# Kernel optimization log

Measured on AMD Instinct MI355X. Metric: run time of the kernel, lower is better.

## Reference

```python
import jax, jax.numpy as jnp
import numpy as np

N = 64
H = 256
B = 32768
OFF = N * (N - 1) // 2  # 2016


def _mlp_params(key, dims, scale_out=0.05):
    ps = []
    for i, (din, dout) in enumerate(zip(dims[:-1], dims[1:])):
        key, k = jax.random.split(key)
        s = 1.0 / np.sqrt(din)
        ps.append((jax.random.normal(k, (dout, din), jnp.float32) * s,
                   jnp.zeros((dout,), jnp.float32)))
    return ps, key


def setup_inputs() -> dict:
    key = jax.random.key(0)
    key, k = jax.random.split(key)
    x = jax.random.normal(k, (B, N), jnp.float32)
    dp, key = _mlp_params(key, [N, H, H, N])
    op, key = _mlp_params(key, [N, H, H, OFF])
    (Wd1, bd1), (Wd2, bd2), (Wdo, bdo) = dp
    (Wo1, bo1), (Wo2, bo2), (Woo, boo) = op
    return {"input": x,
            "Wd1": Wd1, "bd1": bd1, "Wd2": Wd2, "bd2": bd2, "Wdo": Wdo, "bdo": bdo,
            "Wo1": Wo1, "bo1": bo1, "Wo2": Wo2, "bo2": bo2, "Woo": Woo, "boo": boo}


def reference(input, Wd1, bd1, Wd2, bd2, Wdo, bdo, Wo1, bo1, Wo2, bo2, Woo, boo):
    x0 = input  # [B, N]
    # diag branch: tanh MLP -> N diagonal elements per sample
    x = jnp.tanh(input @ Wd1.T + bd1)
    x = jnp.tanh(x @ Wd2.T + bd2)
    x = x @ Wdo.T + bdo  # [B, N]
    # offdiag branch: tanh MLP -> N(N-1)/2 strictly-lower-tri elements
    z = jnp.tanh(input @ Wo1.T + bo1)
    z = jnp.tanh(z @ Wo2.T + bo2)
    z = z @ Woo.T + boo  # [B, OFF]
    n = x.shape[-1]
    b = x0.shape[0]
    rows, cols = np.tril_indices(n, k=-1)  # static index arrays
    diag = np.arange(n)
    L = jnp.zeros((b, n, n), x.dtype)
    L = L.at[:, rows, cols].set(z)
    L = L.at[:, diag, diag].set(x)
    # D[i] = (L L^T) x0[i] computed as L @ (L^T @ x0) to avoid n x n matmul
    y = jnp.einsum('bkj,bk->bj', L, x0)
    D = jnp.einsum('bij,bj->bi', L, y)
    return D
```

## Files before the change

kernel.cpp:

```cpp
#include <hip/hip_runtime.h>
#include <math.h>


#define B_TOT 32768
#define NDIM  64
#define HDIM  256
#define OFFD  2016
#define GRP_UNITS 67584
#define GRP_BYTES 135168

typedef __bf16 bf16x8 __attribute__((ext_vector_type(8)));
typedef float  f32x4  __attribute__((ext_vector_type(4)));

__device__ __forceinline__ float fast_tanh(float x) {
  float e = __expf(2.f * x);
  return 1.f - 2.f * __builtin_amdgcn_rcpf(e + 1.f);
}
__device__ __forceinline__ float lane_bcast(float v, int l) {
  return __uint_as_float(__builtin_amdgcn_readlane(__float_as_uint(v), l));
}
__device__ __forceinline__ float bf_lo(unsigned w) { return __uint_as_float(w << 16); }
__device__ __forceinline__ float bf_hi(unsigned w) { return __uint_as_float(w & 0xffff0000u); }
__device__ __forceinline__ unsigned bfbits(float f) {
  __bf16 h = (__bf16)f;
  return (unsigned)__builtin_bit_cast(unsigned short, h);
}
__device__ __forceinline__ int rs_of(int i) {
  const int a3 = i & 3;
  return ((i * (i - 1)) >> 1) + 6 * (i >> 2) + ((a3 == 2) ? 3 : (a3 == 3) ? 5 : 0);
}

__device__ __forceinline__ void gload_lds16(const void* g, void* l) {
  __builtin_amdgcn_global_load_lds(
      (const __attribute__((address_space(1))) unsigned*)g,
      (__attribute__((address_space(3))) unsigned*)l, 16, 0, 0);
}

#define MFMA(A, B, C) __builtin_amdgcn_mfma_f32_16x16x32_bf16((A), (B), (C), 0, 0, 0)
#define SB0() __builtin_amdgcn_sched_barrier(0)
#define GOFF(g, row) (((((g) & ~7) | (((g) & 7) ^ ((row) & 7)))) << 4)

__device__ __forceinline__ void cast_range(const float* __restrict__ s,
                                           __bf16* __restrict__ d, int n) {
  int i = blockIdx.x * blockDim.x + threadIdx.x;
  const int stride = gridDim.x * blockDim.x;
  for (; i < n; i += stride) d[i] = (__bf16)s[i];
}
__global__ __launch_bounds__(256) void cast_all_kernel(
    const float* s0, __bf16* d0, int n0, const float* s1, __bf16* d1, int n1,
    const float* s2, __bf16* d2, int n2, const float* s3, __bf16* d3, int n3,
    const float* s4, __bf16* d4, int n4, const float* s5, __bf16* d5, int n5,
    __bf16* d6, int n6) {
  cast_range(s0, d0, n0); cast_range(s1, d1, n1); cast_range(s2, d2, n2);
  cast_range(s3, d3, n3); cast_range(s4, d4, n4); cast_range(s5, d5, n5);
  int i = blockIdx.x * blockDim.x + threadIdx.x;
  const int stride = gridDim.x * blockDim.x;
  for (; i < n6; i += stride) d6[i] = (__bf16)0.f;
}

__device__ __forceinline__ bf16x8 cvt8(const float* __restrict__ p) {
  const float4 u = *(const float4*)p;
  const float4 v = *(const float4*)(p + 4);
  bf16x8 r;
  r[0] = (__bf16)u.x; r[1] = (__bf16)u.y; r[2] = (__bf16)u.z; r[3] = (__bf16)u.w;
  r[4] = (__bf16)v.x; r[5] = (__bf16)v.y; r[6] = (__bf16)v.z; r[7] = (__bf16)v.w;
  return r;
}

#define TRK_SMEM (8192 + 32768 + 32768)

__device__ __forceinline__ void stage_chunk2(const char* wreg, char* wb,
                                             int c, int wave) {
  const char* base = wreg + (size_t)c * 16384;
  char* dst = wb + (c & 1) * 16384;
  const int lane = threadIdx.x & 63;
  const int s0 = wave * 64 + lane;
  const int s1 = s0 + 512;
  if (c < 2) {
    const int r0 = s0 >> 3, q0 = (s0 & 7) ^ (r0 & 7);
    gload_lds16(base + r0 * 128 + (q0 << 4), dst + wave * 1024);
    const int r1 = s1 >> 3, q1 = (s1 & 7) ^ (r1 & 7);
    gload_lds16(base + r1 * 128 + (q1 << 4), dst + (wave + 8) * 1024);
  } else {
    const int r0 = s0 >> 5, g0 = s0 & 31;
    const int q0 = (g0 & 24) | ((g0 & 7) ^ (r0 & 7));
    gload_lds16(base + r0 * 512 + (q0 << 4), dst + wave * 1024);
    const int r1 = s1 >> 5, g1 = s1 & 31;
    const int q1 = (g1 & 24) | ((g1 & 7) ^ (r1 & 7));
    gload_lds16(base + r1 * 512 + (q1 << 4), dst + (wave + 8) * 1024);
  }
}

__global__ __launch_bounds__(512, 2) void off_trunk_kernel(
    const float* __restrict__ x, const __bf16* __restrict__ Wreg,
    const float* __restrict__ bo1, const float* __restrict__ bo2,
    __bf16* __restrict__ g2) {
  extern __shared__ char smem[];
  char* xa  = smem;
  char* act = smem + 8192;
  char* wb  = smem + 40960;
  const char* Wc = (const char*)Wreg;

  const int tid = threadIdx.x;
  const int wave = tid >> 6, lane = tid & 63;
  const int lr = lane & 15, lg = lane >> 4;
  const int sb = blockIdx.x * 64;

  float bv1[2], bv2[8];
#pragma unroll
  for (int cc = 0; cc < 2; ++cc) bv1[cc] = bo1[cc * 128 + wave * 16 + lr];
#pragma unroll
  for (int cc = 0; cc < 8; ++cc) bv2[cc] = bo2[cc * 32 + (wave & 1) * 16 + lr];

  {
    const int s = tid >> 3, g = tid & 7;
    const bf16x8 v = cvt8(x + (size_t)(sb + s) * 64 + g * 8);
    *(bf16x8*)(xa + s * 128 + GOFF(g, s)) = v;
  }
  stage_chunk2(Wc, wb, 0, wave);
  __syncthreads();

#pragma unroll
  for (int cc = 0; cc < 2; ++cc) {
    stage_chunk2(Wc, wb, cc + 1, wave);
    const char* wbp = wb + (cc & 1) * 16384;
    const int brow = wave * 16 + lr;
    const bf16x8 b0 = *(const bf16x8*)(wbp + brow * 128 + GOFF(lg, brow));
    const bf16x8 b1 = *(const bf16x8*)(wbp + brow * 128 + GOFF(4 + lg, brow));
    const int ch = cc * 128 + brow;
#pragma unroll
    for (int m = 0; m < 4; ++m) {
      const int arow = m * 16 + lr;
      const bf16x8 a0 = *(const bf16x8*)(xa + arow * 128 + GOFF(lg, arow));
      const bf16x8 a1 = *(const bf16x8*)(xa + arow * 128 + GOFF(4 + lg, arow));
      f32x4 acc = {0.f, 0.f, 0.f, 0.f};
      acc = MFMA(a0, b0, acc);
      acc = MFMA(a1, b1, acc);
#pragma unroll
      for (int r = 0; r < 4; ++r) {
        const int s = m * 16 + lg * 4 + r;
        *(__bf16*)(act + s * 512 + GOFF(ch >> 3, s) + (ch & 7) * 2) =
            (__bf16)fast_tanh(acc[r] + bv1[cc]);
      }
    }
    __syncthreads();
  }

#pragma unroll
  for (int cc = 0; cc < 8; ++cc) {
    const int c = cc + 2;
    if (c + 1 < 10) stage_chunk2(Wc, wb, c + 1, wave);
    const char* wbp = wb + (c & 1) * 16384;
    const int m = wave >> 1, n = wave & 1;
    const int ch = cc * 32 + n * 16 + lr;
    const int brow = n * 16 + lr;
    const int arow = m * 16 + lr;
    f32x4 acc = {0.f, 0.f, 0.f, 0.f};
#pragma unroll
    for (int ks = 0; ks < 8; ++ks) {
      const int g = ks * 4 + lg;
      const bf16x8 a = *(const bf16x8*)(act + arow * 512 + GOFF(g, arow));
      const bf16x8 b = *(const bf16x8*)(wbp + brow * 512 + GOFF(g, brow));
      acc = MFMA(a, b, acc);
    }
#pragma unroll
    for (int r = 0; r < 4; ++r) {
      const int s = m * 16 + lg * 4 + r;
      g2[(size_t)(sb + s) * 256 + ch] = (__bf16)fast_tanh(acc[r] + bv2[cc]);
    }
    if (cc < 7) __syncthreads();
  }
}

__global__ __launch_bounds__(512, 2) void diag_trunk_kernel(
    const float* __restrict__ x, const __bf16* __restrict__ Wreg,
    const float* __restrict__ bd1, const float* __restrict__ bd2,
    const float* __restrict__ bdo, float* __restrict__ xd) {
  extern __shared__ char smem[];
  char* xa  = smem;
  char* act = smem + 8192;
  char* wb  = smem + 40960;
  const char* Wc = (const char*)Wreg;

  const int tid = threadIdx.x;
  const int wave = tid >> 6, lane = tid & 63;
  const int lr = lane & 15, lg = lane >> 4;
  const int sb = blockIdx.x * 64;

  float bv1[2], bv2[8], bv3[2];
#pragma unroll
  for (int cc = 0; cc < 2; ++cc) bv1[cc] = bd1[cc * 128 + wave * 16 + lr];
#pragma unroll
  for (int cc = 0; cc < 8; ++cc) bv2[cc] = bd2[cc * 32 + (wave & 1) * 16 + lr];
#pragma unroll
  for (int cc = 0; cc < 2; ++cc) bv3[cc] = bdo[cc * 32 + (wave & 1) * 16 + lr];

  {
    const int s = tid >> 3, g = tid & 7;
    const bf16x8 v = cvt8(x + (size_t)(sb + s) * 64 + g * 8);
    *(bf16x8*)(xa + s * 128 + GOFF(g, s)) = v;
  }
  stage_chunk2(Wc, wb, 0, wave);
  __syncthreads();

#pragma unroll
  for (int cc = 0; cc < 2; ++cc) {
    stage_chunk2(Wc, wb, cc + 1, wave);
    const char* wbp = wb + (cc & 1) * 16384;
    const int brow = wave * 16 + lr;
    const bf16x8 b0 = *(const bf16x8*)(wbp + brow * 128 + GOFF(lg, brow));
    const bf16x8 b1 = *(const bf16x8*)(wbp + brow * 128 + GOFF(4 + lg, brow));
    const int ch = cc * 128 + brow;
#pragma unroll
    for (int m = 0; m < 4; ++m) {
      const int arow = m * 16 + lr;
      const bf16x8 a0 = *(const bf16x8*)(xa + arow * 128 + GOFF(lg, arow));
      const bf16x8 a1 = *(const bf16x8*)(xa + arow * 128 + GOFF(4 + lg, arow));
      f32x4 acc = {0.f, 0.f, 0.f, 0.f};
      acc = MFMA(a0, b0, acc);
      acc = MFMA(a1, b1, acc);
#pragma unroll
      for (int r = 0; r < 4; ++r) {
        const int s = m * 16 + lg * 4 + r;
        *(__bf16*)(act + s * 512 + GOFF(ch >> 3, s) + (ch & 7) * 2) =
            (__bf16)fast_tanh(acc[r] + bv1[cc]);
      }
    }
    __syncthreads();
  }

  f32x4 h2v[8];
#pragma unroll
  for (int cc = 0; cc < 8; ++cc) {
    const int c = cc + 2;
    if (c + 1 < 11) stage_chunk2(Wc, wb, c + 1, wave);
    const char* wbp = wb + (c & 1) * 16384;
    const int m = wave >> 1, n = wave & 1;
    const int brow = n * 16 + lr;
    const int arow = m * 16 + lr;
    f32x4 acc = {0.f, 0.f, 0.f, 0.f};
#pragma unroll
    for (int ks = 0; ks < 8; ++ks) {
      const int g = ks * 4 + lg;
      const bf16x8 a = *(const bf16x8*)(act + arow * 512 + GOFF(g, arow));
      const bf16x8 b = *(const bf16x8*)(wbp + brow * 512 + GOFF(g, brow));
      acc = MFMA(a, b, acc);
    }
#pragma unroll
    for (int r = 0; r < 4; ++r) h2v[cc][r] = fast_tanh(acc[r] + bv2[cc]);
    __syncthreads();
  }

  {
    const int m = wave >> 1, n = wave & 1;
#pragma unroll
    for (int cc = 0; cc < 8; ++cc) {
      const int ch = cc * 32 + n * 16 + lr;
#pragma unroll
      for (int r = 0; r < 4; ++r) {
        const int s = m * 16 + lg * 4 + r;
        *(__bf16*)(act + s * 512 + GOFF(ch >> 3, s) + (ch & 7) * 2) =
            (__bf16)h2v[cc][r];
      }
    }
  }
  stage_chunk2(Wc, wb, 11, wave);
  __syncthreads();

#pragma unroll
  for (int cc = 0; cc < 2; ++cc) {
    const char* wbp = wb + ((10 + cc) & 1) * 16384;
    const int m = wave >> 1, n = wave & 1;
    const int ch = cc * 32 + n * 16 + lr;
    const int brow = n * 16 + lr;
    const int arow = m * 16 + lr;
    f32x4 acc = {0.f, 0.f, 0.f, 0.f};
#pragma unroll
    for (int ks = 0; ks < 8; ++ks) {
      const int g = ks * 4 + lg;
      const bf16x8 a = *(const bf16x8*)(act + arow * 512 + GOFF(g, arow));
      const bf16x8 b = *(const bf16x8*)(wbp + brow * 512 + GOFF(g, brow));
      acc = MFMA(a, b, acc);
    }
#pragma unroll
    for (int r = 0; r < 4; ++r) {
      const int s = m * 16 + lg * 4 + r;
      xd[(size_t)(sb + s) * 64 + ch] = acc[r] + bv3[cc];
    }
  }
}

#define TILE_BYTES 32768
#define LIST_OFF   131072
#define LIST_CAP   160
#define GEMM_SMEM  (131072 + 1024)

__global__ __launch_bounds__(512, 1) void gemm_z_kernel(
    const __bf16* __restrict__ g2q, const __bf16* __restrict__ Woob,
    const float* __restrict__ boo, __bf16* __restrict__ zq, int bmper) {
  extern __shared__ char gsm[];
  const int tid = threadIdx.x;
  const int wave = tid >> 6, lane = tid & 63;
  const int lr = lane & 15, lg = lane >> 4;
  const int bm = (blockIdx.x & 7) * bmper + (blockIdx.x >> 6);
  const int bn = (blockIdx.x >> 3) & 7;
  const int wr = wave >> 2, wc = wave & 3;
  const int srl = lane >> 3;
  const int sch = lane & 7;

#define STAGE(BUF, KT)                                                          \
  {                                                                             \
    _Pragma("unroll")                                                           \
    for (int j = 0; j < 4; ++j) {                                               \
      const int row = wave * 32 + j * 8 + srl;                                  \
      const int ka = (KT) * 64 + ((sch ^ (row & 7)) << 3);                      \
      gload_lds16(g2q + (size_t)(bm * 256 + row) * 256 + ka,                    \
                  gsm + (BUF) * TILE_BYTES + wave * 4096 + j * 1024);           \
      gload_lds16(Woob + (size_t)(bn * 256 + row) * 256 + ka,                   \
                  gsm + 65536 + (BUF) * TILE_BYTES + wave * 4096 + j * 1024);   \
    }                                                                           \
  }

  int* lcnt = (int*)(gsm + LIST_OFF);
  unsigned* llist = (unsigned*)(gsm + LIST_OFF + 4);
  const int base = bn * 256;

  float bvf[4];
#pragma unroll
  for (int fc = 0; fc < 4; ++fc) {
    const int col = base + wc * 64 + fc * 16 + lr;
    bvf[fc] = (col < OFFD) ? boo[col] : 0.f;
  }

  f32x4 acc[8][4];
#pragma unroll
  for (int i = 0; i < 8; ++i)
#pragma unroll
    for (int j = 0; j < 4; ++j) acc[i][j] = (f32x4){0.f, 0.f, 0.f, 0.f};

  STAGE(0, 0)
  if (tid == 0) *lcnt = 0;
  __syncthreads();

  for (int gi = tid; gi < 528; gi += 512) {
    const int off0 = gi * 4;
    int i = (int)((1.f + sqrtf((float)(8 * off0 + 1))) * 0.5f);
    if (i > 63) i = 63;
    if (i < 1) i = 1;
    while (i > 1 && rs_of(i) > off0) --i;
    while (i < 63 && rs_of(i + 1) <= off0) ++i;
    const int j0 = off0 - rs_of(i);
    int nv = i - j0;
    if (nv > 4) nv = 4;
    const int c0 = ((i * (i - 1)) >> 1) + j0;
    const int last = c0 + nv - 1;
    if (last >= base && c0 <= base + 255) {
      const int idx = atomicAdd(lcnt, 1);
      if (idx < LIST_CAP)
        llist[idx] = ((unsigned)gi << 16) | ((unsigned)i << 9) |
                     ((unsigned)j0 << 3) | (unsigned)nv;
    }
  }
  __syncthreads();

#pragma unroll
  for (int kt = 0; kt < 4; ++kt) {
    if (kt < 3) STAGE((kt + 1) & 1, kt + 1)
    const __bf16* Ab = (const __bf16*)(gsm + (kt & 1) * TILE_BYTES);
    const __bf16* Bb = (const __bf16*)(gsm + 65536 + (kt & 1) * TILE_BYTES);
#pragma unroll
    for (int ks = 0; ks < 2; ++ks) {
      const int cc = ((ks * 4 + lg) ^ (lr & 7)) << 3;
      bf16x8 af[8];
#pragma unroll
      for (int fr = 0; fr < 8; ++fr)
        af[fr] = *(const bf16x8*)(Ab + (wr * 128 + fr * 16 + lr) * 64 + cc);
      bf16x8 bfr[4];
#pragma unroll
      for (int fc = 0; fc < 4; ++fc)
        bfr[fc] = *(const bf16x8*)(Bb + (wc * 64 + fc * 16 + lr) * 64 + cc);
#pragma unroll
      for (int fr = 0; fr < 8; ++fr)
#pragma unroll
        for (int fc = 0; fc < 4; ++fc)
          acc[fr][fc] = MFMA(af[fr], bfr[fc], acc[fr][fc]);
    }
    __syncthreads();
  }

  {
    unsigned long long* Tq = (unsigned long long*)gsm;
#pragma unroll
    for (int fr = 0; fr < 8; ++fr) {
      const int rgrp = wr * 32 + fr * 4 + lg;
#pragma unroll
      for (int fc = 0; fc < 4; ++fc) {
        const int ncol = wc * 64 + fc * 16 + lr;
        const unsigned long long v =
            (unsigned long long)bfbits(acc[fr][fc][0] + bvf[fc]) |
            ((unsigned long long)bfbits(acc[fr][fc][1] + bvf[fc]) << 16) |
            ((unsigned long long)bfbits(acc[fr][fc][2] + bvf[fc]) << 32) |
            ((unsigned long long)bfbits(acc[fr][fc][3] + bvf[fc]) << 48);
        Tq[ncol * 64 + (rgrp ^ (ncol & 7))] = v;
      }
    }
  }
  __syncthreads();

  {
    const unsigned* Tw = (const unsigned*)gsm;
    int nl = *lcnt;
    if (nl > LIST_CAP) nl = LIST_CAP;
    const int p = tid >> 2;
    const int grp = bm * 8 + (p >> 4);
    __bf16* zdst = zq + (size_t)grp * GRP_UNITS + (p & 15) * 4224;
    for (int li = (tid & 3); li < nl; li += 4) {
      const unsigned e = llist[li];
      const int gi = e >> 16;
      const int i = (e >> 9) & 63;
      const int j0 = (e >> 3) & 63;
      const int nv = e & 7;
      const int c0 = ((i * (i - 1)) >> 1) + j0;
      const int lc0 = c0 - base;
      unsigned u[4];
#pragma unroll
      for (int d = 0; d < 4; ++d) {
        const int lc = lc0 + d;
        const bool valid = (d < nv) && (lc >= 0) && (lc <= 255);
        u[d] = valid
                   ? Tw[lc * 128 + (((p >> 1) ^ (lc & 7)) << 1) + (p & 1)]
                   : 0u;
      }
      const bool full = (lc0 >= 0) && (lc0 + nv - 1 <= 255);
      if (full) {
        uint4 w;
        w.x = u[0]; w.y = u[1]; w.z = u[2]; w.w = u[3];
        *(uint4*)(zdst + (size_t)gi * 8) = w;
      } else {
        const bool ownpad = (lc0 + nv - 1 >= 0) && (lc0 + nv - 1 <= 255);
#pragma unroll
        for (int d = 0; d < 4; ++d) {
          const int lc = lc0 + d;
          const bool own =
              (d < nv) ? ((lc >= 0) && (lc <= 255)) : ownpad;
          if (own) *(unsigned*)(zdst + (size_t)gi * 8 + d * 2) = u[d];
        }
      }
    }
  }
}

#define APPLY_SMEM (8 * 8448 + 4096)
__global__ __launch_bounds__(512, 2) void apply_kernel(
    const __bf16* __restrict__ zq, const float* __restrict__ xd,
    const float* __restrict__ x0, float* __restrict__ out, int s0base) {
  extern __shared__ char smem[];
  __bf16* ztb = (__bf16*)smem;
  float* ys2 = (float*)(smem + 8 * 8448);

  const int tid = threadIdx.x;
  const int wave = tid >> 6, lane = tid & 63;
  const int blk = blockIdx.x;
  const int sb = s0base + blk * 16;
  const int s0 = wave * 2, s1 = s0 + 1;

  const float x0vA = x0[(size_t)(sb + s0) * 64 + lane];
  const float x0vB = x0[(size_t)(sb + s1) * 64 + lane];
  const float xdA = xd[(size_t)(sb + s0) * 64 + lane];
  const float xdB = xd[(size_t)(sb + s1) * 64 + lane];

  {
    const char* src = (const char*)zq + (size_t)(blk >> 1) * GRP_BYTES +
                      ((blk & 1) * 8 + wave) * 8448;
    char* dst = smem + wave * 8448;
#pragma unroll
    for (int j = 0; j < 8; ++j)
      gload_lds16(src + j * 1024 + lane * 16, dst + j * 1024);
    if (lane < 16) gload_lds16(src + 8192 + lane * 16, dst + 8192);
  }
  asm volatile("s_waitcnt vmcnt(0)" ::: "memory");
  SB0();

  const __bf16* zpair = ztb + wave * 4224;

  float yA = xdA * x0vA, yB = xdB * x0vB;
  int rs = 0;
#pragma unroll
  for (int k = 1; k < 64; ++k) {
    const unsigned w = *(const unsigned*)(zpair + (rs + lane) * 2);
    const float xkA = lane_bcast(x0vA, k);
    const float xkB = lane_bcast(x0vB, k);
    const bool mvalid = lane < k;
    yA += mvalid ? bf_lo(w) * xkA : 0.f;
    yB += mvalid ? bf_hi(w) * xkB : 0.f;
    rs += (k + 3) & ~3;
  }

  float* yp = ys2 + wave * 128;
  *(float2*)(yp + lane * 2) = make_float2(yA, yB);
  asm volatile("s_waitcnt lgkmcnt(0)" ::: "memory");
  SB0();

  float DA = xdA * yA, DB = xdB * yB;
  float dA1 = 0.f, dB1 = 0.f;
  {
    const int r3 = lane & 3;
    const int rsi = ((lane * (lane - 1)) >> 1) + 6 * (lane >> 2) +
                    ((r3 == 2) ? 3 : (r3 == 3) ? 5 : 0);
    const int cmax = (lane + 3) >> 2;
    const __bf16* zrow = zpair + rsi * 2;
#pragma unroll 4
    for (int c = 0; c < cmax; ++c) {
      const uint4 w = *(const uint4*)(zrow + c * 8);
      const float4 u0 = *(const float4*)(yp + c * 8);
      const float4 u1 = *(const float4*)(yp + c * 8 + 4);
      DA += bf_lo(w.x) * u0.x + bf_lo(w.z) * u1.x;
      dA1 += bf_lo(w.y) * u0.z + bf_lo(w.w) * u1.z;
      DB += bf_hi(w.x) * u0.y + bf_hi(w.z) * u1.y;
      dB1 += bf_hi(w.y) * u0.w + bf_hi(w.w) * u1.w;
    }
  }
  out[(size_t)(sb + s0) * 64 + lane] = DA + dA1;
  out[(size_t)(sb + s1) * 64 + lane] = DB + dB1;
}

extern "C" void kernel_launch(void* const* d_in, const int* in_sizes, int n_in,
                              void* d_out, int out_size, void* d_ws, size_t ws_size,
                              hipStream_t stream) {
  const float* x   = (const float*)d_in[0];
  const float* Wd1 = (const float*)d_in[1];
  const float* bd1 = (const float*)d_in[2];
  const float* Wd2 = (const float*)d_in[3];
  const float* bd2 = (const float*)d_in[4];
  const float* Wdo = (const float*)d_in[5];
  const float* bdo = (const float*)d_in[6];
  const float* Wo1 = (const float*)d_in[7];
  const float* bo1 = (const float*)d_in[8];
  const float* Wo2 = (const float*)d_in[9];
  const float* bo2 = (const float*)d_in[10];
  const float* Woo = (const float*)d_in[11];
  const float* boo = (const float*)d_in[12];
  float* out = (float*)d_out;

  char* ws = (char*)d_ws;
  __bf16* Wcat = (__bf16*)(ws + 0);
  __bf16* Woob = (__bf16*)(ws + 360448);
  __bf16* g2   = (__bf16*)(ws + 1409024);
  float*  xdp  = (float*)(ws + 18186240);
  const size_t zoff = 26574848;
  __bf16* zq   = (__bf16*)(ws + zoff);

  const size_t zcap = (ws_size > zoff) ? (ws_size - zoff) : 0;
  int nslices = 4;
  if (zcap >= (size_t)1024 * GRP_BYTES) nslices = 1;
  else if (zcap >= (size_t)512 * GRP_BYTES) nslices = 2;
  const int QSs = B_TOT / nslices;
  const int nbm = QSs / 256;
  const int bmper = nbm >> 3;

  cast_all_kernel<<<512, 256, 0, stream>>>(
      Wo1, Wcat, HDIM * NDIM,
      Wo2, Wcat + 16384, HDIM * HDIM,
      Wd1, Wcat + 81920, HDIM * NDIM,
      Wd2, Wcat + 98304, HDIM * HDIM,
      Wdo, Wcat + 163840, NDIM * HDIM,
      Woo, Woob, OFFD * HDIM,
      Woob + OFFD * HDIM, 32 * HDIM);

  hipFuncSetAttribute((const void*)off_trunk_kernel,
                      hipFuncAttributeMaxDynamicSharedMemorySize, TRK_SMEM);
  hipFuncSetAttribute((const void*)diag_trunk_kernel,
                      hipFuncAttributeMaxDynamicSharedMemorySize, TRK_SMEM);
  off_trunk_kernel<<<B_TOT / 64, 512, TRK_SMEM, stream>>>(
      x, Wcat, bo1, bo2, g2);
  diag_trunk_kernel<<<B_TOT / 64, 512, TRK_SMEM, stream>>>(
      x, Wcat + 81920, bd1, bd2, bdo, xdp);

  hipFuncSetAttribute((const void*)gemm_z_kernel,
                      hipFuncAttributeMaxDynamicSharedMemorySize, GEMM_SMEM);
  hipFuncSetAttribute((const void*)apply_kernel,
                      hipFuncAttributeMaxDynamicSharedMemorySize, APPLY_SMEM);
  for (int s = 0; s < nslices; ++s) {
    gemm_z_kernel<<<nbm * 8, 512, GEMM_SMEM, stream>>>(
        g2 + (size_t)s * QSs * HDIM, Woob, boo, zq, bmper);
    apply_kernel<<<QSs / 16, 512, APPLY_SMEM, stream>>>(zq, xdp, x, out, s * QSs);
  }
}
```

Measured before the change: 154.0 us.

## Shrink z-GEMM tiles to 128x128 with single-buffered LDS for higher occupancy

The off-diagonal output GEMM moves from 256x256 tiles with 512 threads and double-buffered LDS (about 129KB) to 128x128 tiles with 256 threads and a single 32KB LDS buffer, allowing up to four blocks per CU. The grid grows to 16 column tiles per row tile, and the epilogue transpose and list-based scatter are re-indexed for the smaller tile. The aim is more resident waves to hide latency, at the cost of losing the prefetch overlap, adding a barrier per k-step, and re-reading operands more often from global memory.

New measurement: 154.8 us. No clear change (+0.5%).

```diff
diff --git a/kernel.cpp b/kernel.cpp
--- a/kernel.cpp
+++ b/kernel.cpp
@@ -290,40 +290,38 @@
   }
 }
 
-#define TILE_BYTES 32768
-#define LIST_OFF   131072
-#define LIST_CAP   160
-#define GEMM_SMEM  (131072 + 1024)
-
-__global__ __launch_bounds__(512, 1) void gemm_z_kernel(
+#define LIST_OFF 32768
+#define LIST_CAP 160
+#define GZ_SMEM  (32768 + 1024)
+
+__global__ __launch_bounds__(256, 4) void gemm_z_kernel(
     const __bf16* __restrict__ g2q, const __bf16* __restrict__ Woob,
     const float* __restrict__ boo, __bf16* __restrict__ zq, int bmper) {
   extern __shared__ char gsm[];
   const int tid = threadIdx.x;
   const int wave = tid >> 6, lane = tid & 63;
   const int lr = lane & 15, lg = lane >> 4;
-  const int bm = (blockIdx.x & 7) * bmper + (blockIdx.x >> 6);
-  const int bn = (blockIdx.x >> 3) & 7;
-  const int wr = wave >> 2, wc = wave & 3;
-  const int srl = lane >> 3;
-  const int sch = lane & 7;
-
-#define STAGE(BUF, KT)                                                          \
+  const int bm = (blockIdx.x & 7) * bmper + (blockIdx.x >> 7);
+  const int bn = (blockIdx.x >> 3) & 15;
+  const int wr = wave >> 1, wc = wave & 1;
+  const int srl = lane >> 3, sch = lane & 7;
+
+  int* lcnt = (int*)(gsm + LIST_OFF);
+  unsigned* llist = (unsigned*)(gsm + LIST_OFF + 4);
+  const int base = bn * 128;
+
+#define GZSTAGE(KT)                                                             \
   {                                                                             \
     _Pragma("unroll")                                                           \
     for (int j = 0; j < 4; ++j) {                                               \
       const int row = wave * 32 + j * 8 + srl;                                  \
       const int ka = (KT) * 64 + ((sch ^ (row & 7)) << 3);                      \
-      gload_lds16(g2q + (size_t)(bm * 256 + row) * 256 + ka,                    \
-                  gsm + (BUF) * TILE_BYTES + wave * 4096 + j * 1024);           \
-      gload_lds16(Woob + (size_t)(bn * 256 + row) * 256 + ka,                   \
-                  gsm + 65536 + (BUF) * TILE_BYTES + wave * 4096 + j * 1024);   \
+      gload_lds16(g2q + (size_t)(bm * 128 + row) * 256 + ka,                    \
+                  gsm + wave * 4096 + j * 1024);                                \
+      gload_lds16(Woob + (size_t)(bn * 128 + row) * 256 + ka,                   \
+                  gsm + 16384 + wave * 4096 + j * 1024);                        \
     }                                                                           \
   }
-
-  int* lcnt = (int*)(gsm + LIST_OFF);
-  unsigned* llist = (unsigned*)(gsm + LIST_OFF + 4);
-  const int base = bn * 256;
 
   float bvf[4];
 #pragma unroll
@@ -332,17 +330,17 @@
     bvf[fc] = (col < OFFD) ? boo[col] : 0.f;
   }
 
-  f32x4 acc[8][4];
-#pragma unroll
-  for (int i = 0; i < 8; ++i)
+  f32x4 acc[4][4];
+#pragma unroll
+  for (int i = 0; i < 4; ++i)
 #pragma unroll
     for (int j = 0; j < 4; ++j) acc[i][j] = (f32x4){0.f, 0.f, 0.f, 0.f};
 
-  STAGE(0, 0)
+  GZSTAGE(0)
   if (tid == 0) *lcnt = 0;
   __syncthreads();
 
-  for (int gi = tid; gi < 528; gi += 512) {
+  for (int gi = tid; gi < 528; gi += 256) {
     const int off0 = gi * 4;
     int i = (int)((1.f + sqrtf((float)(8 * off0 + 1))) * 0.5f);
     if (i > 63) i = 63;
@@ -354,33 +352,34 @@
     if (nv > 4) nv = 4;
     const int c0 = ((i * (i - 1)) >> 1) + j0;
     const int last = c0 + nv - 1;
-    if (last >= base && c0 <= base + 255) {
+    if (last >= base && c0 <= base + 127) {
       const int idx = atomicAdd(lcnt, 1);
       if (idx < LIST_CAP)
         llist[idx] = ((unsigned)gi << 16) | ((unsigned)i << 9) |
                      ((unsigned)j0 << 3) | (unsigned)nv;
     }
   }
-  __syncthreads();
 
 #pragma unroll
   for (int kt = 0; kt < 4; ++kt) {
-    if (kt < 3) STAGE((kt + 1) & 1, kt + 1)
-    const __bf16* Ab = (const __bf16*)(gsm + (kt & 1) * TILE_BYTES);
-    const __bf16* Bb = (const __bf16*)(gsm + 65536 + (kt & 1) * TILE_BYTES);
+    if (kt > 0) {
+      GZSTAGE(kt)
+      __syncthreads();
+    }
+    const __bf16* Ab = (const __bf16*)gsm;
+    const __bf16* Bb = (const __bf16*)(gsm + 16384);
 #pragma unroll
     for (int ks = 0; ks < 2; ++ks) {
-      const int cc = ((ks * 4 + lg) ^ (lr & 7)) << 3;
-      bf16x8 af[8];
-#pragma unroll
-      for (int fr = 0; fr < 8; ++fr)
-        af[fr] = *(const bf16x8*)(Ab + (wr * 128 + fr * 16 + lr) * 64 + cc);
-      bf16x8 bfr[4];
-#pragma unroll
-      for (int fc = 0; fc < 4; ++fc)
-        bfr[fc] = *(const bf16x8*)(Bb + (wc * 64 + fc * 16 + lr) * 64 + cc);
-#pragma unroll
-      for (int fr = 0; fr < 8; ++fr)
+      bf16x8 af[4], bfr[4];
+#pragma unroll
+      for (int f = 0; f < 4; ++f) {
+        const int ra = wr * 64 + f * 16 + lr;
+        af[f] = *(const bf16x8*)((const char*)Ab + ra * 128 + GOFF(ks * 4 + lg, ra));
+        const int rb = wc * 64 + f * 16 + lr;
+        bfr[f] = *(const bf16x8*)((const char*)Bb + rb * 128 + GOFF(ks * 4 + lg, rb));
+      }
+#pragma unroll
+      for (int fr = 0; fr < 4; ++fr)
 #pragma unroll
         for (int fc = 0; fc < 4; ++fc)
           acc[fr][fc] = MFMA(af[fr], bfr[fc], acc[fr][fc]);
@@ -391,8 +390,8 @@
   {
     unsigned long long* Tq = (unsigned long long*)gsm;
 #pragma unroll
-    for (int fr = 0; fr < 8; ++fr) {
-      const int rgrp = wr * 32 + fr * 4 + lg;
+    for (int fr = 0; fr < 4; ++fr) {
+      const int rgrp = wr * 16 + fr * 4 + lg;
 #pragma unroll
       for (int fc = 0; fc < 4; ++fc) {
         const int ncol = wc * 64 + fc * 16 + lr;
@@ -401,7 +400,7 @@
             ((unsigned long long)bfbits(acc[fr][fc][1] + bvf[fc]) << 16) |
             ((unsigned long long)bfbits(acc[fr][fc][2] + bvf[fc]) << 32) |
             ((unsigned long long)bfbits(acc[fr][fc][3] + bvf[fc]) << 48);
-        Tq[ncol * 64 + (rgrp ^ (ncol & 7))] = v;
+        Tq[ncol * 32 + (rgrp ^ (ncol & 7))] = v;
       }
     }
   }
@@ -412,7 +411,7 @@
     int nl = *lcnt;
     if (nl > LIST_CAP) nl = LIST_CAP;
     const int p = tid >> 2;
-    const int grp = bm * 8 + (p >> 4);
+    const int grp = bm * 4 + (p >> 4);
     __bf16* zdst = zq + (size_t)grp * GRP_UNITS + (p & 15) * 4224;
     for (int li = (tid & 3); li < nl; li += 4) {
       const unsigned e = llist[li];
@@ -426,23 +425,23 @@
 #pragma unroll
       for (int d = 0; d < 4; ++d) {
         const int lc = lc0 + d;
-        const bool valid = (d < nv) && (lc >= 0) && (lc <= 255);
+        const bool valid = (d < nv) && (lc >= 0) && (lc <= 127);
         u[d] = valid
-                   ? Tw[lc * 128 + (((p >> 1) ^ (lc & 7)) << 1) + (p & 1)]
+                   ? Tw[lc * 64 + (((p >> 1) ^ (lc & 7)) << 1) + (p & 1)]
                    : 0u;
       }
-      const bool full = (lc0 >= 0) && (lc0 + nv - 1 <= 255);
+      const bool full = (lc0 >= 0) && (lc0 + nv - 1 <= 127);
       if (full) {
         uint4 w;
         w.x = u[0]; w.y = u[1]; w.z = u[2]; w.w = u[3];
         *(uint4*)(zdst + (size_t)gi * 8) = w;
       } else {
-        const bool ownpad = (lc0 + nv - 1 >= 0) && (lc0 + nv - 1 <= 255);
+        const bool ownpad = (lc0 + nv - 1 >= 0) && (lc0 + nv - 1 <= 127);
 #pragma unroll
         for (int d = 0; d < 4; ++d) {
           const int lc = lc0 + d;
           const bool own =
-              (d < nv) ? ((lc >= 0) && (lc <= 255)) : ownpad;
+              (d < nv) ? ((lc >= 0) && (lc <= 127)) : ownpad;
           if (own) *(unsigned*)(zdst + (size_t)gi * 8 + d * 2) = u[d];
         }
       }
@@ -555,7 +554,7 @@
   if (zcap >= (size_t)1024 * GRP_BYTES) nslices = 1;
   else if (zcap >= (size_t)512 * GRP_BYTES) nslices = 2;
   const int QSs = B_TOT / nslices;
-  const int nbm = QSs / 256;
+  const int nbm = QSs / 128;
   const int bmper = nbm >> 3;
 
   cast_all_kernel<<<512, 256, 0, stream>>>(
@@ -577,11 +576,11 @@
       x, Wcat + 81920, bd1, bd2, bdo, xdp);
 
   hipFuncSetAttribute((const void*)gemm_z_kernel,
-                      hipFuncAttributeMaxDynamicSharedMemorySize, GEMM_SMEM);
+                      hipFuncAttributeMaxDynamicSharedMemorySize, GZ_SMEM);
   hipFuncSetAttribute((const void*)apply_kernel,
                       hipFuncAttributeMaxDynamicSharedMemorySize, APPLY_SMEM);
   for (int s = 0; s < nslices; ++s) {
-    gemm_z_kernel<<<nbm * 8, 512, GEMM_SMEM, stream>>>(
+    gemm_z_kernel<<<nbm * 16, 256, GZ_SMEM, stream>>>(
         g2 + (size_t)s * QSs * HDIM, Woob, boo, zq, bmper);
     apply_kernel<<<QSs / 16, 512, APPLY_SMEM, stream>>>(zq, xdp, x, out, s * QSs);
   }
```
